# Optimization experiments

Measured on AMD Instinct MI355X. Metric: run time of the kernel, lower is better.

## Reference

```python
import jax, jax.numpy as jnp
import numpy as np

ANCHOR_STRIDE = 16
BASE_SIZE = 16
RATIOS = np.array([0.5, 1.0, 2.0])
SCALES = np.array([8.0, 16.0, 32.0])
RPN_NEG = 0.3
RPN_POS = 0.7
RPN_BATCH = 256
FG_FRAC = 0.5


def _generate_anchors():
    w = h = float(BASE_SIZE)
    cx = cy = 0.5 * (BASE_SIZE - 1)
    size = w * h
    ws = np.round(np.sqrt(size / RATIOS))
    hs = np.round(ws * RATIOS)
    out = []
    for wi, hi in zip(ws, hs):
        wss = wi * SCALES
        hss = hi * SCALES
        out.append(np.stack([cx - 0.5 * (wss - 1), cy - 0.5 * (hss - 1),
                             cx + 0.5 * (wss - 1), cy + 0.5 * (hss - 1)], 1))
    return np.concatenate(out, 0).astype(np.float32)  # [9, 4]


def _all_anchors(height, width):
    anchors = _generate_anchors()  # [A,4]
    sx = np.arange(width) * ANCHOR_STRIDE
    sy = np.arange(height) * ANCHOR_STRIDE
    SX, SY = np.meshgrid(sx, sy)  # 'xy' -> [H,W], row-major y then x
    shifts = np.stack([SX.ravel(), SY.ravel(), SX.ravel(), SY.ravel()], 1).astype(np.float32)  # [K,4]
    return (shifts[:, None, :] + anchors[None, :, :]).reshape(-1, 4), anchors.shape[0]  # [K*A,4], A


def _iou(a, g):
    # a: [N,4], g: [G,4]; +1 pixel convention
    area_a = (a[:, 2] - a[:, 0] + 1.0) * (a[:, 3] - a[:, 1] + 1.0)
    area_g = (g[:, 2] - g[:, 0] + 1.0) * (g[:, 3] - g[:, 1] + 1.0)
    iw = jnp.clip(jnp.minimum(a[:, None, 2], g[None, :, 2]) - jnp.maximum(a[:, None, 0], g[None, :, 0]) + 1.0, 0.0)
    ih = jnp.clip(jnp.minimum(a[:, None, 3], g[None, :, 3]) - jnp.maximum(a[:, None, 1], g[None, :, 1]) + 1.0, 0.0)
    inter = iw * ih  # [N,G]
    return inter / (area_a[:, None] + area_g[None, :] - inter)


def _bbox_transform(a, g):
    aw = a[:, 2] - a[:, 0] + 1.0
    ah = a[:, 3] - a[:, 1] + 1.0
    acx = a[:, 0] + 0.5 * (aw - 1.0)
    acy = a[:, 1] + 0.5 * (ah - 1.0)
    gw = g[:, 2] - g[:, 0] + 1.0
    gh = g[:, 3] - g[:, 1] + 1.0
    gcx = g[:, 0] + 0.5 * (gw - 1.0)
    gcy = g[:, 1] + 0.5 * (gh - 1.0)
    return jnp.stack([(gcx - acx) / aw, (gcy - acy) / ah, jnp.log(gw / aw), jnp.log(gh / ah)], 1)


def setup_inputs() -> dict:
    key = jax.random.key(0)
    B, G, H, W = 32, 50, 64, 64
    img = ANCHOR_STRIDE * H  # 1024
    k1, k2, k3, k4 = jax.random.split(key, 4)
    x1 = jax.random.uniform(k1, (B * G,)) * (img - 224.0)
    y1 = jax.random.uniform(k2, (B * G,)) * (img - 224.0)
    bw = 16.0 + jax.random.uniform(k3, (B * G,)) * 180.0
    bh = 16.0 + jax.random.uniform(k4, (B * G,)) * 180.0
    gt_bbox = jnp.stack([x1, y1, x1 + bw, y1 + bh], 1)
    return {"gt_bbox": gt_bbox, "batch_size": B, "n_gt": G, "height": H, "width": W}


def reference(gt_bbox, batch_size, n_gt, height, width):
    all_a, A = _all_anchors(height, width)
    img_w = ANCHOR_STRIDE * width
    img_h = ANCHOR_STRIDE * height
    inside = np.where((all_a[:, 0] >= 0) & (all_a[:, 1] >= 0) &
                      (all_a[:, 2] < img_w) & (all_a[:, 3] < img_h))[0]
    anc = jnp.asarray(all_a[inside])  # [N,4], static subset
    N = len(inside)
    NUM_FG = int(FG_FRAC * RPN_BATCH)
    gt = gt_bbox.reshape(batch_size, n_gt, 4)

    def subsample(mask, num_keep, k):
        # keep a random subset of size <= num_keep among mask==True
        pri = jnp.where(mask, jax.random.uniform(k, (N,)), jnp.inf)
        order = jnp.argsort(pri)
        rank = jnp.zeros((N,), jnp.int32).at[order].set(jnp.arange(N, dtype=jnp.int32))
        return mask & (rank < num_keep)

    def per_image(gt_b, key):
        ov = _iou(anc, gt_b)                 # [N,G]
        max_ov = ov.max(1)
        arg = ov.argmax(1)
        gt_max = ov.max(0)                   # [G]
        labels = jnp.full((N,), -1.0)
        labels = jnp.where(max_ov < RPN_NEG, 0.0, labels)
        labels = jnp.where(max_ov >= RPN_POS, 1.0, labels)
        # anchors achieving per-gt max overlap (for gts with positive overlap)
        gt_arg_hit = ((ov == gt_max[None, :]) & (gt_max[None, :] > 0)).any(1)
        labels = jnp.where(gt_arg_hit, 1.0, labels)
        kf, kb = jax.random.split(key)
        fg = labels == 1.0
        keep_fg = subsample(fg, NUM_FG, kf)
        labels = jnp.where(fg & ~keep_fg, -1.0, labels)
        num_bg = RPN_BATCH - keep_fg.sum()
        bg = labels == 0.0
        keep_bg = subsample(bg, num_bg, kb)
        labels = jnp.where(bg & ~keep_bg, -1.0, labels)
        reg = _bbox_transform(anc, gt_b[arg]) * jnp.clip(labels, 0.0)[:, None]
        return labels, reg

    keys = jax.random.split(jax.random.key(42), batch_size)
    labels, reg = jax.vmap(per_image)(gt, keys)  # [B,N], [B,N,4]

    KA = all_a.shape[0]
    all_labels = jnp.full((batch_size, KA), -1.0).at[:, inside].set(labels)
    all_reg = jnp.zeros((batch_size, KA, 4)).at[:, inside].set(reg)
    all_labels = all_labels.reshape(batch_size, height, width, A).transpose(0, 3, 1, 2)
    all_reg = all_reg.reshape(batch_size, height, width, A * 4).transpose(0, 3, 1, 2)
    return all_labels, all_reg
```

## Files before the change

### kernel.cpp

```cpp
#include <hip/hip_runtime.h>

#pragma clang fp contract(off)

#define BB 32
#define GG 50
#define AA 9
#define HH 64
#define WW 64
#define KAT (HH*WW*AA)
#define NCAP 23552
#define MAXC 4096
#define NUMFG 128
#define RPNB 256
#define BG_T 0.05f
#define LAB_SZ (BB*AA*HH*WW)
#define NGTB (BB*GG)
#define NMSKB 72
#define NPREPB (KAT/256)
#define NBLK4 23

__constant__ float c_aw[9] = {184.f,368.f,736.f,128.f,256.f,512.f, 88.f,176.f,352.f};
__constant__ float c_ah[9] = { 96.f,192.f,384.f,128.f,256.f,512.f,176.f,352.f,704.f};
__constant__ int c_xlo[9] = {6,11,23,4,8,16,3,5,11};
__constant__ int c_xhi[9] = {57,52,40,59,55,47,60,58,52};
__constant__ int c_nx [9] = {52,42,18,56,48,32,58,54,42};
__constant__ int c_ylo[9] = {3,6,12,4,8,16,5,11,22};
__constant__ int c_yhi[9] = {60,57,51,59,55,47,58,52,41};
__constant__ int c_ny [9] = {58,52,40,56,48,32,54,42,20};
__constant__ int c_pb[9] = {0,3072,6144,7168,11264,14336,15360,19456,22528};
__constant__ int c_fb[9] = {0,3,6,7,11,14,15,19,22};
__constant__ int c_bt4[NBLK4] = {0,0,0,1,1,1,2,3,3,3,3,4,4,4,5,6,6,6,6,7,7,7,8};

__device__ __forceinline__ unsigned rotl32(unsigned v, int d) {
  return (v << d) | (v >> (32 - d));
}

__device__ __forceinline__ void tf2x32(unsigned k0, unsigned k1,
                                       unsigned x0, unsigned x1,
                                       unsigned &o0, unsigned &o1) {
  unsigned ks2 = k0 ^ k1 ^ 0x1BD11BDAu;
  x0 += k0; x1 += k1;
#define TF_R(r) { x0 += x1; x1 = rotl32(x1, (r)); x1 ^= x0; }
  TF_R(13) TF_R(15) TF_R(26) TF_R(6)
  x0 += k1;  x1 += ks2 + 1u;
  TF_R(17) TF_R(29) TF_R(16) TF_R(24)
  x0 += ks2; x1 += k0 + 2u;
  TF_R(13) TF_R(15) TF_R(26) TF_R(6)
  x0 += k0;  x1 += k1 + 3u;
  TF_R(17) TF_R(29) TF_R(16) TF_R(24)
  x0 += k1;  x1 += ks2 + 4u;
  TF_R(13) TF_R(15) TF_R(26) TF_R(6)
  x0 += ks2; x1 += k0 + 5u;
#undef TF_R
  o0 = x0; o1 = x1;
}

__device__ __forceinline__ float bits_to_uniform(unsigned bits) {
  return __uint_as_float((bits >> 9) | 0x3f800000u) - 1.0f;
}

__device__ __forceinline__ float pri_uniform(unsigned k0, unsigned k1, int i) {
  unsigned o0, o1;
  tf2x32(k0, k1, 0u, (unsigned)i, o0, o1);
  return bits_to_uniform(o0 ^ o1);
}

__device__ __forceinline__ void box_from_ayx(int a, int x, int y,
                                             float &ax1, float &ay1, float &ax2, float &ay2) {
  float hw = 0.5f * (c_aw[a] - 1.0f);
  float hh = 0.5f * (c_ah[a] - 1.0f);
  float cx = (float)(16 * x) + 7.5f;
  float cy = (float)(16 * y) + 7.5f;
  ax1 = cx - hw; ay1 = cy - hh; ax2 = cx + hw; ay2 = cy + hh;
}

__device__ __forceinline__ void divmod_nx(int t, int rc, int &q, int &rm) {
  switch (t) {
    case 0: q = rc / 52; rm = rc - q * 52; break;
    case 1: q = rc / 42; rm = rc - q * 42; break;
    case 2: q = rc / 18; rm = rc - q * 18; break;
    case 3: q = rc / 56; rm = rc - q * 56; break;
    case 4: q = rc / 48; rm = rc - q * 48; break;
    case 5: q = rc / 32; rm = rc - q * 32; break;
    case 6: q = rc / 58; rm = rc - q * 58; break;
    case 7: q = rc / 54; rm = rc - q * 54; break;
    default: q = rc / 42; rm = rc - q * 42; break;
  }
}

__global__ void __launch_bounds__(256) k_pg(
    const float* __restrict__ gt,
    unsigned* __restrict__ keyf, unsigned* __restrict__ keyb,
    int* __restrict__ fg_cnt, int* __restrict__ bg_cnt,
    float* __restrict__ gt_max, unsigned long long* __restrict__ gmask,
    int* __restrict__ iref_j) {
  if (blockIdx.x == NGTB) {
    if (threadIdx.x < BB) {
      int b = threadIdx.x;
      fg_cnt[b] = 0; bg_cnt[b] = 0;
      unsigned h, l, f0, f1, g0, g1;
      tf2x32(0u, 42u, 0u, (unsigned)b, h, l);
      tf2x32(h, l, 0u, 0u, f0, f1);
      tf2x32(h, l, 0u, 1u, g0, g1);
      keyf[2*b] = f0; keyf[2*b+1] = f1;
      keyb[2*b] = g0; keyb[2*b+1] = g1;
    }
    return;
  }
  if (blockIdx.x > NGTB && blockIdx.x <= NGTB + NMSKB) {
    int idx = blockIdx.x - NGTB - 1;
    int pair = idx * 4 + (threadIdx.x >> 6);
    int b = pair / AA, t = pair % AA;
    int y = threadIdx.x & 63;
    float hh = 0.5f * (c_ah[t] - 1.0f);
    float cy = (float)(16 * y) + 7.5f;
    float ay1 = cy - hh, ay2 = cy + hh;
    unsigned long long m = 0;
    for (int g = 0; g < GG; ++g) {
      float gy1 = gt[(b * GG + g) * 4 + 1];
      float gy2 = gt[(b * GG + g) * 4 + 3];
      float ih = (fminf(ay2, gy2) - fmaxf(ay1, gy1)) + 1.0f;
      if (ih > 0.0f) m |= (1ull << g);
    }
    gmask[(b * AA + t) * 64 + y] = m;
    return;
  }
  if (blockIdx.x > NGTB + NMSKB) {
    int ka = (blockIdx.x - NGTB - 1 - NMSKB) * 256 + threadIdx.x;
    int a = ka % AA, pos = ka / AA, x = pos & 63, y = pos >> 6;
    int pre = 0; bool mine = false;
#pragma unroll
    for (int tt = 0; tt < 9; ++tt) {
      int xlo = c_xlo[tt], xhi = c_xhi[tt], ylo = c_ylo[tt], yhi = c_yhi[tt];
      int rb = min(y, yhi + 1) - ylo; rb = max(rb, 0);
      pre += c_nx[tt] * rb;
      if (y >= ylo && y <= yhi) {
        int cb = min(x, xhi + 1) - xlo; cb = max(cb, 0);
        pre += cb;
        bool ins = (x >= xlo) && (x <= xhi);
        if (ins && tt < a) pre++;
        if (tt == a) mine = ins;
      }
    }
    if (mine) {
      int j = c_pb[a] + (y - c_ylo[a]) * c_nx[a] + (x - c_xlo[a]);
      iref_j[j] = pre;
    }
    return;
  }
  int b = blockIdx.x / GG, g = blockIdx.x % GG;
  const float* gr = gt + (b * GG + g) * 4;
  float gx1 = gr[0], gy1 = gr[1], gx2 = gr[2], gy2 = gr[3];
  float gar = ((gx2 - gx1) + 1.0f) * ((gy2 - gy1) + 1.0f);
  int lane = threadIdx.x & 63, wv = threadIdx.x >> 6;
  float best = 0.0f;
#pragma unroll
  for (int t = 0; t < 9; ++t) {
    float hw = 0.5f * (c_aw[t] - 1.0f), hh = 0.5f * (c_ah[t] - 1.0f);
    int x0 = max(c_xlo[t], (int)floorf((gx1 - 8.5f - hw) * 0.0625f) - 1);
    int x1 = min(c_xhi[t], (int)ceilf ((gx2 - 6.5f + hw) * 0.0625f) + 1);
    int y0 = max(c_ylo[t], (int)floorf((gy1 - 8.5f - hh) * 0.0625f) - 1);
    int y1 = min(c_yhi[t], (int)ceilf ((gy2 - 6.5f + hh) * 0.0625f) + 1);
    if (x1 < x0 || y1 < y0) continue;
    int x = min(x0 + lane, x1);
    float cx = (float)(16 * x) + 7.5f;
    float ax1 = cx - hw, ax2 = cx + hw;
    float aarv = ((ax2 - ax1) + 1.0f) * ((hh + hh) + 1.0f);
    float iw = (fminf(ax2, gx2) - fmaxf(ax1, gx1)) + 1.0f; iw = fmaxf(iw, 0.0f);
    for (int y = y0 + wv; y <= y1; y += 4) {
      float cy = (float)(16 * y) + 7.5f;
      float ay1 = cy - hh, ay2 = cy + hh;
      float ih = (fminf(ay2, gy2) - fmaxf(ay1, gy1)) + 1.0f; ih = fmaxf(ih, 0.0f);
      float inter = iw * ih;
      best = fmaxf(best, inter / ((aarv + gar) - inter));
    }
  }
  for (int off = 32; off > 0; off >>= 1)
    best = fmaxf(best, __shfl_down(best, off));
  __shared__ float red[4];
  if (lane == 0) red[wv] = best;
  __syncthreads();
  if (threadIdx.x == 0)
    gt_max[b * GG + g] = fmaxf(fmaxf(red[0], red[1]), fmaxf(red[2], red[3]));
}

__global__ void __launch_bounds__(256) k_labels(
    const float* __restrict__ gt, const float* __restrict__ gt_max,
    const unsigned long long* __restrict__ gmask, const int* __restrict__ iref_j,
    const unsigned* __restrict__ keyf, const unsigned* __restrict__ keyb,
    signed char* __restrict__ lab, unsigned char* __restrict__ am,
    int* __restrict__ fg_cnt, unsigned long long* __restrict__ fg_key, int* __restrict__ fg_j,
    int* __restrict__ bg_cnt, unsigned long long* __restrict__ bg_key, int* __restrict__ bg_j) {
  __shared__ float4 sbox[GG];
  __shared__ float2 sga[GG];
  __shared__ unsigned long long s_gm[64];
  __shared__ unsigned long long s_fgk[1024]; __shared__ int s_fgj[1024];
  __shared__ unsigned long long s_bgk[1024]; __shared__ int s_bgj[1024];
  __shared__ int s_fgc, s_bgc, s_fgbase, s_bgbase;
  int b = blockIdx.y;
  int t = c_bt4[blockIdx.x];
  if (threadIdx.x == 0) { s_fgc = 0; s_bgc = 0; }
  if (threadIdx.x < GG) {
    float4 gbx = ((const float4*)(gt + b * GG * 4))[threadIdx.x];
    sbox[threadIdx.x] = gbx;
    float gar = ((gbx.z - gbx.x) + 1.0f) * ((gbx.w - gbx.y) + 1.0f);
    float m = gt_max[b * GG + threadIdx.x];
    sga[threadIdx.x] = make_float2(gar, (m > 0.0f) ? m : -1.0f);
  }
  if (threadIdx.x >= 64 && threadIdx.x < 128)
    s_gm[threadIdx.x - 64] = gmask[(b * AA + t) * 64 + (threadIdx.x - 64)];
  __syncthreads();

  int nx = c_nx[t];
  int nxny = nx * c_ny[t];
  int lane = threadIdx.x & 63, wv = threadIdx.x >> 6;
  int wstart = (blockIdx.x - c_fb[t]) * 1024 + wv * 256;

  float AX1[4], AY1[4], AX2[4], AY2[4], AV[4], BEST[4];
  int ARG[4]; bool ACT[4], HIT[4];
#pragma unroll
  for (int k = 0; k < 4; ++k) {
    int r = wstart + k * 64 + lane;
    ACT[k] = r < nxny;
    int rc = min(r, nxny - 1);
    int yy, xx; divmod_nx(t, rc, yy, xx);
    box_from_ayx(t, c_xlo[t] + xx, c_ylo[t] + yy, AX1[k], AY1[k], AX2[k], AY2[k]);
    AV[k] = ((AX2[k] - AX1[k]) + 1.0f) * ((AY2[k] - AY1[k]) + 1.0f);
    BEST[k] = 0.0f; ARG[k] = 0; HIT[k] = false;
  }

  unsigned long long m = 0;
  if (wstart < nxny) {
    int y0, y1, dum;
    divmod_nx(t, wstart, y0, dum);
    divmod_nx(t, min(wstart + 255, nxny - 1), y1, dum);
    int yy = y0 + lane;
    unsigned long long rowm = (yy <= y1) ? s_gm[c_ylo[t] + yy] : 0ull;
    unsigned lo = (unsigned)rowm, hi = (unsigned)(rowm >> 32);
    for (int off = 32; off > 0; off >>= 1) {
      lo |= (unsigned)__shfl_xor((int)lo, off);
      hi |= (unsigned)__shfl_xor((int)hi, off);
    }
    unsigned mlo = (unsigned)__builtin_amdgcn_readfirstlane((int)lo);
    unsigned mhi = (unsigned)__builtin_amdgcn_readfirstlane((int)hi);
    m = (((unsigned long long)mhi << 32) | (unsigned long long)mlo)
        & ((1ull << GG) - 1ull);
  }

  if (m) {
    int g = __builtin_ctzll(m); m &= m - 1;
    float4 gb = sbox[g]; float2 ga = sga[g];
    for (;;) {
      bool more = (m != 0ull);
      int g2 = 0; float4 gb2 = gb; float2 ga2 = ga;
      if (more) {
        g2 = __builtin_ctzll(m); m &= m - 1;
        gb2 = sbox[g2]; ga2 = sga[g2];
      }
#pragma unroll
      for (int k = 0; k < 4; ++k) {
        float iw = (fminf(AX2[k], gb.z) - fmaxf(AX1[k], gb.x)) + 1.0f; iw = fmaxf(iw, 0.0f);
        float ih = (fminf(AY2[k], gb.w) - fmaxf(AY1[k], gb.y)) + 1.0f; ih = fmaxf(ih, 0.0f);
        float inter = iw * ih;
        float ov = inter / ((AV[k] + ga.x) - inter);
        if (ov > BEST[k]) { BEST[k] = ov; ARG[k] = g; }
        HIT[k] = HIT[k] || (ov == ga.y);
      }
      if (!more) break;
      g = g2; gb = gb2; ga = ga2;
    }
  }

#pragma unroll
  for (int k = 0; k < 4; ++k) {
    int label = (HIT[k] || BEST[k] >= 0.7f) ? 1 : ((BEST[k] < 0.3f) ? 0 : -1);
    int j = c_pb[t] + wstart + k * 64 + lane;
    if (ACT[k]) {
      lab[b * NCAP + j] = (signed char)label;
      am[b * NCAP + j]  = (unsigned char)ARG[k];
    }
    int ir = ACT[k] ? iref_j[j] : 0;
    bool wf = ACT[k] && (label == 1);
    unsigned long long mf = __ballot(wf);
    if (mf) {
      int ldr = __builtin_ctzll(mf);
      int basew = 0;
      if (lane == ldr) basew = atomicAdd(&s_fgc, __popcll(mf));
      basew = __shfl(basew, ldr);
      if (wf) {
        float p = pri_uniform(keyf[2*b], keyf[2*b+1], ir);
        int pos = basew + __popcll(mf & ((1ull << lane) - 1ull));
        s_fgk[pos] = ((unsigned long long)__float_as_uint(p) << 32) | (unsigned)ir;
        s_fgj[pos] = j;
      }
    }
    float pb = 0.0f;
    bool wb = ACT[k] && (label == 0);
    if (wb) { pb = pri_uniform(keyb[2*b], keyb[2*b+1], ir); wb = (pb < BG_T); }
    unsigned long long mb = __ballot(wb);
    if (mb) {
      int ldr = __builtin_ctzll(mb);
      int basew = 0;
      if (lane == ldr) basew = atomicAdd(&s_bgc, __popcll(mb));
      basew = __shfl(basew, ldr);
      if (wb) {
        int pos = basew + __popcll(mb & ((1ull << lane) - 1ull));
        s_bgk[pos] = ((unsigned long long)__float_as_uint(pb) << 32) | (unsigned)ir;
        s_bgj[pos] = j;
      }
    }
  }
  __syncthreads();
  if (threadIdx.x == 0) s_fgbase = s_fgc ? atomicAdd(&fg_cnt[b], s_fgc) : 0;
  if (threadIdx.x == 64) s_bgbase = s_bgc ? atomicAdd(&bg_cnt[b], s_bgc) : 0;
  __syncthreads();
  for (int i = threadIdx.x; i < s_fgc; i += 256) {
    int pos = s_fgbase + i;
    if (pos < MAXC) { fg_key[b * MAXC + pos] = s_fgk[i]; fg_j[b * MAXC + pos] = s_fgj[i]; }
  }
  for (int i = threadIdx.x; i < s_bgc; i += 256) {
    int pos = s_bgbase + i;
    if (pos < MAXC) { bg_key[b * MAXC + pos] = s_bgk[i]; bg_j[b * MAXC + pos] = s_bgj[i]; }
  }
}

__global__ void __launch_bounds__(1024) k_select(
    const int* __restrict__ fg_cnt, const unsigned long long* __restrict__ fg_key,
    const int* __restrict__ fg_j,
    const int* __restrict__ bg_cnt, const unsigned long long* __restrict__ bg_key,
    const int* __restrict__ bg_j,
    signed char* __restrict__ lab) {
  __shared__ unsigned long long sk[MAXC];
  __shared__ int sj[MAXC];
  int b = blockIdx.x & (BB - 1);
  if (blockIdx.x < BB) {
    int F = min(fg_cnt[b], MAXC);
    if (F <= NUMFG) return;
    for (int c = threadIdx.x; c < F; c += blockDim.x) {
      sk[c] = fg_key[b * MAXC + c]; sj[c] = fg_j[b * MAXC + c];
    }
    __syncthreads();
    for (int c = threadIdx.x; c < F; c += blockDim.x) {
      unsigned long long me = sk[c];
      int rank = 0;
      for (int jx = 0; jx < F; ++jx) rank += (sk[jx] < me) ? 1 : 0;
      if (rank >= NUMFG) lab[b * NCAP + sj[c]] = -1;
    }
  } else {
    int nk = RPNB - min(fg_cnt[b], NUMFG);
    int C = min(bg_cnt[b], MAXC);
    for (int c = threadIdx.x; c < C; c += blockDim.x) {
      sk[c] = bg_key[b * MAXC + c]; sj[c] = bg_j[b * MAXC + c];
    }
    __syncthreads();
    for (int c = threadIdx.x; c < C; c += blockDim.x) {
      unsigned long long me = sk[c];
      int rank = 0;
      for (int jx = 0; jx < C; ++jx) rank += (sk[jx] < me) ? 1 : 0;
      if (rank < nk) lab[b * NCAP + sj[c]] = 2;
    }
  }
}

__global__ void k_out(const float* __restrict__ gt,
                      const signed char* __restrict__ lab, const unsigned char* __restrict__ am,
                      float* __restrict__ out) {
  int b = blockIdx.y;
  int t = blockIdx.x * 256 + threadIdx.x;
  int a = t >> 12, pos = t & 4095;
  int y = pos >> 6, x = pos & 63;
  int j = -1;
  if (x >= c_xlo[a] && x <= c_xhi[a] && y >= c_ylo[a] && y <= c_yhi[a])
    j = c_pb[a] + (y - c_ylo[a]) * c_nx[a] + (x - c_xlo[a]);
  float lv = -1.0f, t0 = 0.f, t1 = 0.f, t2 = 0.f, t3 = 0.f;
  if (j >= 0) {
    signed char v = lab[b * NCAP + j];
    lv = (v == 1) ? 1.0f : ((v == 2) ? 0.0f : -1.0f);
    if (v == 1) {
      float ax1, ay1, ax2, ay2;
      box_from_ayx(a, x, y, ax1, ay1, ax2, ay2);
      int g = am[b * NCAP + j];
      const float* gr = gt + (b * GG + g) * 4;
      float gx1 = gr[0], gy1 = gr[1], gx2 = gr[2], gy2 = gr[3];
      float aw = (ax2 - ax1) + 1.0f, ah = (ay2 - ay1) + 1.0f;
      float acx = ax1 + 0.5f * (aw - 1.0f), acy = ay1 + 0.5f * (ah - 1.0f);
      float gw = (gx2 - gx1) + 1.0f, gh = (gy2 - gy1) + 1.0f;
      float gcx = gx1 + 0.5f * (gw - 1.0f), gcy = gy1 + 0.5f * (gh - 1.0f);
      t0 = (gcx - acx) / aw;
      t1 = (gcy - acy) / ah;
      t2 = logf(gw / aw);
      t3 = logf(gh / ah);
    }
  }
  out[b * KAT + t] = lv;
  float* rb = out + LAB_SZ + b * (4 * KAT) + (a * 4) * 4096 + pos;
  rb[0] = t0; rb[4096] = t1; rb[2 * 4096] = t2; rb[3 * 4096] = t3;
}

extern "C" void kernel_launch(void* const* d_in, const int* in_sizes, int n_in,
                              void* d_out, int out_size, void* d_ws, size_t ws_size,
                              hipStream_t stream) {
  const float* gt = (const float*)d_in[0];
  float* out = (float*)d_out;

  char* w = (char*)d_ws;
  unsigned long long* fg_key = (unsigned long long*)w; w += BB*MAXC*8;
  unsigned long long* bg_key = (unsigned long long*)w; w += BB*MAXC*8;
  unsigned long long* gmask  = (unsigned long long*)w; w += BB*AA*64*8;
  int* iref_j      = (int*)w;            w += NCAP*sizeof(int);
  int* fg_cnt      = (int*)w;            w += 256;
  int* bg_cnt      = (int*)w;            w += 256;
  unsigned* keyf   = (unsigned*)w;       w += 256;
  unsigned* keyb   = (unsigned*)w;       w += 256;
  float* gt_max    = (float*)w;          w += ((BB*GG*4 + 255)/256)*256;
  int* fg_j        = (int*)w;            w += BB*MAXC*sizeof(int);
  int* bg_j        = (int*)w;            w += BB*MAXC*sizeof(int);
  signed char* lab = (signed char*)w;    w += BB*NCAP;
  unsigned char* am= (unsigned char*)w;  w += BB*NCAP;

  k_pg<<<NGTB + 1 + NMSKB + NPREPB, 256, 0, stream>>>(gt, keyf, keyb, fg_cnt, bg_cnt,
                                                      gt_max, gmask, iref_j);
  k_labels<<<dim3(NBLK4, BB), 256, 0, stream>>>(gt, gt_max, gmask, iref_j, keyf, keyb,
                                                lab, am, fg_cnt, fg_key, fg_j,
                                                bg_cnt, bg_key, bg_j);
  k_select<<<2*BB, 1024, 0, stream>>>(fg_cnt, fg_key, fg_j, bg_cnt, bg_key, bg_j, lab);
  k_out<<<dim3(KAT/256, BB), 256, 0, stream>>>(gt, lab, am, out);
}
```

Before: 150.9 us.

## Fuse four pipeline kernels into one cooperative persistent kernel with grid syncs

Replaces four separate kernel launches with a single cooperative persistent kernel of 1024 blocks. Each stage runs as a role over virtual block indices and the stages are separated by grid.sync(), which removes launch gaps between kernels. The select stage also moves from 64 blocks of 1024 threads to 256 blocks of 256 threads, each block ranking a quarter of the candidates, and drops the shared index array. The fused kernel holds a fixed 32KB of shared memory per block, which can limit occupancy, and a fallback to separate launches runs if the cooperative launch fails.

```diff
diff --git a/kernel.cpp b/kernel.cpp
--- a/kernel.cpp
+++ b/kernel.cpp
@@ -1,6 +1,9 @@
 #include <hip/hip_runtime.h>
+#include <hip/hip_cooperative_groups.h>
 
 #pragma clang fp contract(off)
+
+namespace cg = cooperative_groups;
 
 #define BB 32
 #define GG 50
@@ -18,6 +21,13 @@
 #define NMSKB 72
 #define NPREPB (KAT/256)
 #define NBLK4 23
+#define NV0 (NGTB + 1 + NMSKB + NPREPB)
+#define NV1 (NBLK4*BB)
+#define NV2 (BB*8)
+#define NV3 ((KAT/256)*BB)
+#define GRID 1024
+#define LBL_SMEM 26304
+#define SEL_SMEM 32768
 
 __constant__ float c_aw[9] = {184.f,368.f,736.f,128.f,256.f,512.f, 88.f,176.f,352.f};
 __constant__ float c_ah[9] = { 96.f,192.f,384.f,128.f,256.f,512.f,176.f,352.f,704.f};
@@ -88,13 +98,11 @@
   }
 }
 
-__global__ void __launch_bounds__(256) k_pg(
-    const float* __restrict__ gt,
-    unsigned* __restrict__ keyf, unsigned* __restrict__ keyb,
-    int* __restrict__ fg_cnt, int* __restrict__ bg_cnt,
-    float* __restrict__ gt_max, unsigned long long* __restrict__ gmask,
-    int* __restrict__ iref_j) {
-  if (blockIdx.x == NGTB) {
+
+__device__ __forceinline__ void role_p0(int vb, const float* __restrict__ gt,
+    unsigned* keyf, unsigned* keyb, int* fg_cnt, int* bg_cnt,
+    float* gt_max, unsigned long long* gmask, int* iref_j, char* smem) {
+  if (vb == NGTB) {
     if (threadIdx.x < BB) {
       int b = threadIdx.x;
       fg_cnt[b] = 0; bg_cnt[b] = 0;
@@ -107,8 +115,8 @@
     }
     return;
   }
-  if (blockIdx.x > NGTB && blockIdx.x <= NGTB + NMSKB) {
-    int idx = blockIdx.x - NGTB - 1;
+  if (vb > NGTB && vb <= NGTB + NMSKB) {
+    int idx = vb - NGTB - 1;
     int pair = idx * 4 + (threadIdx.x >> 6);
     int b = pair / AA, t = pair % AA;
     int y = threadIdx.x & 63;
@@ -125,8 +133,8 @@
     gmask[(b * AA + t) * 64 + y] = m;
     return;
   }
-  if (blockIdx.x > NGTB + NMSKB) {
-    int ka = (blockIdx.x - NGTB - 1 - NMSKB) * 256 + threadIdx.x;
+  if (vb > NGTB + NMSKB) {
+    int ka = (vb - NGTB - 1 - NMSKB) * 256 + threadIdx.x;
     int a = ka % AA, pos = ka / AA, x = pos & 63, y = pos >> 6;
     int pre = 0; bool mine = false;
 #pragma unroll
@@ -148,7 +156,7 @@
     }
     return;
   }
-  int b = blockIdx.x / GG, g = blockIdx.x % GG;
+  int b = vb / GG, g = vb % GG;
   const float* gr = gt + (b * GG + g) * 4;
   float gx1 = gr[0], gy1 = gr[1], gx2 = gr[2], gy2 = gr[3];
   float gar = ((gx2 - gx1) + 1.0f) * ((gy2 - gy1) + 1.0f);
@@ -177,29 +185,32 @@
   }
   for (int off = 32; off > 0; off >>= 1)
     best = fmaxf(best, __shfl_down(best, off));
-  __shared__ float red[4];
+  float* red = (float*)smem;
   if (lane == 0) red[wv] = best;
   __syncthreads();
   if (threadIdx.x == 0)
     gt_max[b * GG + g] = fmaxf(fmaxf(red[0], red[1]), fmaxf(red[2], red[3]));
-}
-
-__global__ void __launch_bounds__(256) k_labels(
-    const float* __restrict__ gt, const float* __restrict__ gt_max,
-    const unsigned long long* __restrict__ gmask, const int* __restrict__ iref_j,
+  __syncthreads();
+}
+
+__device__ __forceinline__ void role_labels(int vb, const float* __restrict__ gt,
+    const float* __restrict__ gt_max, const unsigned long long* __restrict__ gmask,
+    const int* __restrict__ iref_j,
     const unsigned* __restrict__ keyf, const unsigned* __restrict__ keyb,
     signed char* __restrict__ lab, unsigned char* __restrict__ am,
-    int* __restrict__ fg_cnt, unsigned long long* __restrict__ fg_key, int* __restrict__ fg_j,
-    int* __restrict__ bg_cnt, unsigned long long* __restrict__ bg_key, int* __restrict__ bg_j) {
-  __shared__ float4 sbox[GG];
-  __shared__ float2 sga[GG];
-  __shared__ unsigned long long s_gm[64];
-  __shared__ unsigned long long s_fgk[1024]; __shared__ int s_fgj[1024];
-  __shared__ unsigned long long s_bgk[1024]; __shared__ int s_bgj[1024];
-  __shared__ int s_fgc, s_bgc, s_fgbase, s_bgbase;
-  int b = blockIdx.y;
-  int t = c_bt4[blockIdx.x];
-  if (threadIdx.x == 0) { s_fgc = 0; s_bgc = 0; }
+    int* fg_cnt, unsigned long long* fg_key, int* fg_j,
+    int* bg_cnt, unsigned long long* bg_key, int* bg_j, char* smem) {
+  int b = vb / NBLK4, bx = vb - b * NBLK4;
+  int t = c_bt4[bx];
+  float4* sbox = (float4*)smem;
+  float2* sga  = (float2*)(smem + 800);
+  unsigned long long* s_gm  = (unsigned long long*)(smem + 1200);
+  unsigned long long* s_fgk = (unsigned long long*)(smem + 1712);
+  int* s_fgj = (int*)(smem + 9904);
+  unsigned long long* s_bgk = (unsigned long long*)(smem + 14000);
+  int* s_bgj = (int*)(smem + 22192);
+  int* s_cnt = (int*)(smem + 26288);
+  if (threadIdx.x == 0) { s_cnt[0] = 0; s_cnt[1] = 0; }
   if (threadIdx.x < GG) {
     float4 gbx = ((const float4*)(gt + b * GG * 4))[threadIdx.x];
     sbox[threadIdx.x] = gbx;
@@ -211,10 +222,9 @@
     s_gm[threadIdx.x - 64] = gmask[(b * AA + t) * 64 + (threadIdx.x - 64)];
   __syncthreads();
 
-  int nx = c_nx[t];
-  int nxny = nx * c_ny[t];
+  int nxny = c_nx[t] * c_ny[t];
   int lane = threadIdx.x & 63, wv = threadIdx.x >> 6;
-  int wstart = (blockIdx.x - c_fb[t]) * 1024 + wv * 256;
+  int wstart = (bx - c_fb[t]) * 1024 + wv * 256;
 
   float AX1[4], AY1[4], AX2[4], AY2[4], AV[4], BEST[4];
   int ARG[4]; bool ACT[4], HIT[4];
@@ -285,7 +295,7 @@
     if (mf) {
       int ldr = __builtin_ctzll(mf);
       int basew = 0;
-      if (lane == ldr) basew = atomicAdd(&s_fgc, __popcll(mf));
+      if (lane == ldr) basew = atomicAdd(&s_cnt[0], __popcll(mf));
       basew = __shfl(basew, ldr);
       if (wf) {
         float p = pri_uniform(keyf[2*b], keyf[2*b+1], ir);
@@ -301,7 +311,7 @@
     if (mb) {
       int ldr = __builtin_ctzll(mb);
       int basew = 0;
-      if (lane == ldr) basew = atomicAdd(&s_bgc, __popcll(mb));
+      if (lane == ldr) basew = atomicAdd(&s_cnt[1], __popcll(mb));
       basew = __shfl(basew, ldr);
       if (wb) {
         int pos = basew + __popcll(mb & ((1ull << lane) - 1ull));
@@ -311,62 +321,62 @@
     }
   }
   __syncthreads();
-  if (threadIdx.x == 0) s_fgbase = s_fgc ? atomicAdd(&fg_cnt[b], s_fgc) : 0;
-  if (threadIdx.x == 64) s_bgbase = s_bgc ? atomicAdd(&bg_cnt[b], s_bgc) : 0;
-  __syncthreads();
-  for (int i = threadIdx.x; i < s_fgc; i += 256) {
-    int pos = s_fgbase + i;
+  if (threadIdx.x == 0) s_cnt[2] = s_cnt[0] ? atomicAdd(&fg_cnt[b], s_cnt[0]) : 0;
+  if (threadIdx.x == 64) s_cnt[3] = s_cnt[1] ? atomicAdd(&bg_cnt[b], s_cnt[1]) : 0;
+  __syncthreads();
+  int fgc = s_cnt[0], bgc = s_cnt[1], fgb = s_cnt[2], bgb = s_cnt[3];
+  for (int i = threadIdx.x; i < fgc; i += 256) {
+    int pos = fgb + i;
     if (pos < MAXC) { fg_key[b * MAXC + pos] = s_fgk[i]; fg_j[b * MAXC + pos] = s_fgj[i]; }
   }
-  for (int i = threadIdx.x; i < s_bgc; i += 256) {
-    int pos = s_bgbase + i;
+  for (int i = threadIdx.x; i < bgc; i += 256) {
+    int pos = bgb + i;
     if (pos < MAXC) { bg_key[b * MAXC + pos] = s_bgk[i]; bg_j[b * MAXC + pos] = s_bgj[i]; }
   }
-}
-
-__global__ void __launch_bounds__(1024) k_select(
+  __syncthreads();
+}
+
+__device__ __forceinline__ void role_select(int vb,
     const int* __restrict__ fg_cnt, const unsigned long long* __restrict__ fg_key,
     const int* __restrict__ fg_j,
     const int* __restrict__ bg_cnt, const unsigned long long* __restrict__ bg_key,
     const int* __restrict__ bg_j,
-    signed char* __restrict__ lab) {
-  __shared__ unsigned long long sk[MAXC];
-  __shared__ int sj[MAXC];
-  int b = blockIdx.x & (BB - 1);
-  if (blockIdx.x < BB) {
-    int F = min(fg_cnt[b], MAXC);
-    if (F <= NUMFG) return;
-    for (int c = threadIdx.x; c < F; c += blockDim.x) {
-      sk[c] = fg_key[b * MAXC + c]; sj[c] = fg_j[b * MAXC + c];
-    }
+    signed char* __restrict__ lab, char* smem) {
+  int img = vb >> 3, slot = vb & 7;
+  unsigned long long* sk = (unsigned long long*)smem;
+  if (slot < 4) {
+    int F = min(fg_cnt[img], MAXC);
+    if (F > NUMFG) {
+      for (int i = threadIdx.x; i < F; i += 256) sk[i] = fg_key[img * MAXC + i];
+      __syncthreads();
+      for (int c = slot * 256 + threadIdx.x; c < F; c += 1024) {
+        unsigned long long me = sk[c];
+        int rank = 0;
+        for (int jx = 0; jx < F; ++jx) rank += (sk[jx] < me) ? 1 : 0;
+        if (rank >= NUMFG) lab[img * NCAP + fg_j[img * MAXC + c]] = -1;
+      }
+    }
+  } else {
+    int sub = slot - 4;
+    int nk = RPNB - min(fg_cnt[img], NUMFG);
+    int C = min(bg_cnt[img], MAXC);
+    for (int i = threadIdx.x; i < C; i += 256) sk[i] = bg_key[img * MAXC + i];
     __syncthreads();
-    for (int c = threadIdx.x; c < F; c += blockDim.x) {
-      unsigned long long me = sk[c];
-      int rank = 0;
-      for (int jx = 0; jx < F; ++jx) rank += (sk[jx] < me) ? 1 : 0;
-      if (rank >= NUMFG) lab[b * NCAP + sj[c]] = -1;
-    }
-  } else {
-    int nk = RPNB - min(fg_cnt[b], NUMFG);
-    int C = min(bg_cnt[b], MAXC);
-    for (int c = threadIdx.x; c < C; c += blockDim.x) {
-      sk[c] = bg_key[b * MAXC + c]; sj[c] = bg_j[b * MAXC + c];
-    }
-    __syncthreads();
-    for (int c = threadIdx.x; c < C; c += blockDim.x) {
+    for (int c = sub * 256 + threadIdx.x; c < C; c += 1024) {
       unsigned long long me = sk[c];
       int rank = 0;
       for (int jx = 0; jx < C; ++jx) rank += (sk[jx] < me) ? 1 : 0;
-      if (rank < nk) lab[b * NCAP + sj[c]] = 2;
-    }
-  }
-}
-
-__global__ void k_out(const float* __restrict__ gt,
-                      const signed char* __restrict__ lab, const unsigned char* __restrict__ am,
-                      float* __restrict__ out) {
-  int b = blockIdx.y;
-  int t = blockIdx.x * 256 + threadIdx.x;
+      if (rank < nk) lab[img * NCAP + bg_j[img * MAXC + c]] = 2;
+    }
+  }
+  __syncthreads();
+}
+
+__device__ __forceinline__ void role_out(int vb, const float* __restrict__ gt,
+    const signed char* __restrict__ lab, const unsigned char* __restrict__ am,
+    float* __restrict__ out) {
+  int b = vb / (KAT/256), bx = vb - b * (KAT/256);
+  int t = bx * 256 + threadIdx.x;
   int a = t >> 12, pos = t & 4095;
   int y = pos >> 6, x = pos & 63;
   int j = -1;
@@ -397,6 +407,60 @@
   rb[0] = t0; rb[4096] = t1; rb[2 * 4096] = t2; rb[3 * 4096] = t3;
 }
 
+extern "C" __global__ void __launch_bounds__(256, 4) k_fused(
+    const float* __restrict__ gt, float* __restrict__ out,
+    unsigned* keyf, unsigned* keyb, int* fg_cnt, int* bg_cnt,
+    float* gt_max, unsigned long long* gmask, int* iref_j,
+    unsigned long long* fg_key, int* fg_j,
+    unsigned long long* bg_key, int* bg_j,
+    signed char* lab, unsigned char* am) {
+  cg::grid_group grid = cg::this_grid();
+  __shared__ __align__(16) char smem[SEL_SMEM];
+  for (int vb = blockIdx.x; vb < NV0; vb += GRID)
+    role_p0(vb, gt, keyf, keyb, fg_cnt, bg_cnt, gt_max, gmask, iref_j, smem);
+  grid.sync();
+  for (int vb = blockIdx.x; vb < NV1; vb += GRID)
+    role_labels(vb, gt, gt_max, gmask, iref_j, keyf, keyb, lab, am,
+                fg_cnt, fg_key, fg_j, bg_cnt, bg_key, bg_j, smem);
+  grid.sync();
+  for (int vb = blockIdx.x; vb < NV2; vb += GRID)
+    role_select(vb, fg_cnt, fg_key, fg_j, bg_cnt, bg_key, bg_j, lab, smem);
+  grid.sync();
+  for (int vb = blockIdx.x; vb < NV3; vb += GRID)
+    role_out(vb, gt, lab, am, out);
+}
+
+__global__ void __launch_bounds__(256) k_p0_fb(const float* __restrict__ gt,
+    unsigned* keyf, unsigned* keyb, int* fg_cnt, int* bg_cnt,
+    float* gt_max, unsigned long long* gmask, int* iref_j) {
+  __shared__ __align__(16) char smem[64];
+  role_p0(blockIdx.x, gt, keyf, keyb, fg_cnt, bg_cnt, gt_max, gmask, iref_j, smem);
+}
+__global__ void __launch_bounds__(256) k_lab_fb(const float* __restrict__ gt,
+    const float* __restrict__ gt_max, const unsigned long long* __restrict__ gmask,
+    const int* __restrict__ iref_j,
+    const unsigned* __restrict__ keyf, const unsigned* __restrict__ keyb,
+    signed char* lab, unsigned char* am,
+    int* fg_cnt, unsigned long long* fg_key, int* fg_j,
+    int* bg_cnt, unsigned long long* bg_key, int* bg_j) {
+  __shared__ __align__(16) char smem[LBL_SMEM];
+  role_labels(blockIdx.x, gt, gt_max, gmask, iref_j, keyf, keyb, lab, am,
+              fg_cnt, fg_key, fg_j, bg_cnt, bg_key, bg_j, smem);
+}
+__global__ void __launch_bounds__(256) k_sel_fb(
+    const int* __restrict__ fg_cnt, const unsigned long long* __restrict__ fg_key,
+    const int* __restrict__ fg_j,
+    const int* __restrict__ bg_cnt, const unsigned long long* __restrict__ bg_key,
+    const int* __restrict__ bg_j, signed char* lab) {
+  __shared__ __align__(16) char smem[SEL_SMEM];
+  role_select(blockIdx.x, fg_cnt, fg_key, fg_j, bg_cnt, bg_key, bg_j, lab, smem);
+}
+__global__ void __launch_bounds__(256) k_out_fb(const float* __restrict__ gt,
+    const signed char* __restrict__ lab, const unsigned char* __restrict__ am,
+    float* __restrict__ out) {
+  role_out(blockIdx.x, gt, lab, am, out);
+}
+
 extern "C" void kernel_launch(void* const* d_in, const int* in_sizes, int n_in,
                               void* d_out, int out_size, void* d_ws, size_t ws_size,
                               hipStream_t stream) {
@@ -418,11 +482,19 @@
   signed char* lab = (signed char*)w;    w += BB*NCAP;
   unsigned char* am= (unsigned char*)w;  w += BB*NCAP;
 
-  k_pg<<<NGTB + 1 + NMSKB + NPREPB, 256, 0, stream>>>(gt, keyf, keyb, fg_cnt, bg_cnt,
-                                                      gt_max, gmask, iref_j);
-  k_labels<<<dim3(NBLK4, BB), 256, 0, stream>>>(gt, gt_max, gmask, iref_j, keyf, keyb,
-                                                lab, am, fg_cnt, fg_key, fg_j,
-                                                bg_cnt, bg_key, bg_j);
-  k_select<<<2*BB, 1024, 0, stream>>>(fg_cnt, fg_key, fg_j, bg_cnt, bg_key, bg_j, lab);
-  k_out<<<dim3(KAT/256, BB), 256, 0, stream>>>(gt, lab, am, out);
-}
+  void* args[] = { (void*)&gt, (void*)&out, (void*)&keyf, (void*)&keyb,
+                   (void*)&fg_cnt, (void*)&bg_cnt, (void*)&gt_max, (void*)&gmask,
+                   (void*)&iref_j, (void*)&fg_key, (void*)&fg_j,
+                   (void*)&bg_key, (void*)&bg_j, (void*)&lab, (void*)&am };
+  hipError_t e = hipLaunchCooperativeKernel((void*)k_fused, dim3(GRID), dim3(256),
+                                            args, 0, stream);
+  if (e != hipSuccess) {
+    k_p0_fb<<<NV0, 256, 0, stream>>>(gt, keyf, keyb, fg_cnt, bg_cnt,
+                                     gt_max, gmask, iref_j);
+    k_lab_fb<<<NV1, 256, 0, stream>>>(gt, gt_max, gmask, iref_j, keyf, keyb,
+                                      lab, am, fg_cnt, fg_key, fg_j,
+                                      bg_cnt, bg_key, bg_j);
+    k_sel_fb<<<NV2, 256, 0, stream>>>(fg_cnt, fg_key, fg_j, bg_cnt, bg_key, bg_j, lab);
+    k_out_fb<<<NV3, 256, 0, stream>>>(gt, lab, am, out);
+  }
+}
```

New measurement: 466.5 us. 209% more time.

## Split per-image rank selection across eight 256-thread blocks per image

Applied to the files above, without the earlier changes.

k_select now launches eight 256-thread blocks per image instead of two 1024-thread blocks. Four blocks handle foreground and four handle background, and each covers a strided slice of candidates while every block reloads the full key array into shared memory. The j-index array is read from global memory only when a write is needed, which drops its shared copy. k_labels is also switched to a flattened 1D grid. The aim is to spread the quadratic rank loop over more CUs, at the cost of loading the keys four times per image.

```diff
diff --git a/kernel.cpp b/kernel.cpp
--- a/kernel.cpp
+++ b/kernel.cpp
@@ -18,6 +18,12 @@
 #define NMSKB 72
 #define NPREPB (KAT/256)
 #define NBLK4 23
+#define NV0 (NGTB + 1 + NMSKB + NPREPB)
+#define NV1 (NBLK4*BB)
+#define NV2 (BB*8)
+#define NV3 ((KAT/256)*BB)
+#define LBL_SMEM 26304
+#define SEL_SMEM 32768
 
 __constant__ float c_aw[9] = {184.f,368.f,736.f,128.f,256.f,512.f, 88.f,176.f,352.f};
 __constant__ float c_ah[9] = { 96.f,192.f,384.f,128.f,256.f,512.f,176.f,352.f,704.f};
@@ -197,8 +203,8 @@
   __shared__ unsigned long long s_fgk[1024]; __shared__ int s_fgj[1024];
   __shared__ unsigned long long s_bgk[1024]; __shared__ int s_bgj[1024];
   __shared__ int s_fgc, s_bgc, s_fgbase, s_bgbase;
-  int b = blockIdx.y;
-  int t = c_bt4[blockIdx.x];
+  int b = blockIdx.x / NBLK4, bx = blockIdx.x - b * NBLK4;
+  int t = c_bt4[bx];
   if (threadIdx.x == 0) { s_fgc = 0; s_bgc = 0; }
   if (threadIdx.x < GG) {
     float4 gbx = ((const float4*)(gt + b * GG * 4))[threadIdx.x];
@@ -211,10 +217,9 @@
     s_gm[threadIdx.x - 64] = gmask[(b * AA + t) * 64 + (threadIdx.x - 64)];
   __syncthreads();
 
-  int nx = c_nx[t];
-  int nxny = nx * c_ny[t];
+  int nxny = c_nx[t] * c_ny[t];
   int lane = threadIdx.x & 63, wv = threadIdx.x >> 6;
-  int wstart = (blockIdx.x - c_fb[t]) * 1024 + wv * 256;
+  int wstart = (bx - c_fb[t]) * 1024 + wv * 256;
 
   float AX1[4], AY1[4], AX2[4], AY2[4], AV[4], BEST[4];
   int ARG[4]; bool ACT[4], HIT[4];
@@ -324,47 +329,43 @@
   }
 }
 
-__global__ void __launch_bounds__(1024) k_select(
+__global__ void __launch_bounds__(256) k_select(
     const int* __restrict__ fg_cnt, const unsigned long long* __restrict__ fg_key,
     const int* __restrict__ fg_j,
     const int* __restrict__ bg_cnt, const unsigned long long* __restrict__ bg_key,
     const int* __restrict__ bg_j,
     signed char* __restrict__ lab) {
   __shared__ unsigned long long sk[MAXC];
-  __shared__ int sj[MAXC];
-  int b = blockIdx.x & (BB - 1);
-  if (blockIdx.x < BB) {
-    int F = min(fg_cnt[b], MAXC);
+  int img = blockIdx.x >> 3, slot = blockIdx.x & 7;
+  if (slot < 4) {
+    int F = min(fg_cnt[img], MAXC);
     if (F <= NUMFG) return;
-    for (int c = threadIdx.x; c < F; c += blockDim.x) {
-      sk[c] = fg_key[b * MAXC + c]; sj[c] = fg_j[b * MAXC + c];
-    }
+    for (int i = threadIdx.x; i < F; i += 256) sk[i] = fg_key[img * MAXC + i];
     __syncthreads();
-    for (int c = threadIdx.x; c < F; c += blockDim.x) {
+    for (int c = slot * 256 + threadIdx.x; c < F; c += 1024) {
       unsigned long long me = sk[c];
       int rank = 0;
       for (int jx = 0; jx < F; ++jx) rank += (sk[jx] < me) ? 1 : 0;
-      if (rank >= NUMFG) lab[b * NCAP + sj[c]] = -1;
+      if (rank >= NUMFG) lab[img * NCAP + fg_j[img * MAXC + c]] = -1;
     }
   } else {
-    int nk = RPNB - min(fg_cnt[b], NUMFG);
-    int C = min(bg_cnt[b], MAXC);
-    for (int c = threadIdx.x; c < C; c += blockDim.x) {
-      sk[c] = bg_key[b * MAXC + c]; sj[c] = bg_j[b * MAXC + c];
-    }
+    int sub = slot - 4;
+    int nk = RPNB - min(fg_cnt[img], NUMFG);
+    int C = min(bg_cnt[img], MAXC);
+    for (int i = threadIdx.x; i < C; i += 256) sk[i] = bg_key[img * MAXC + i];
     __syncthreads();
-    for (int c = threadIdx.x; c < C; c += blockDim.x) {
+    for (int c = sub * 256 + threadIdx.x; c < C; c += 1024) {
       unsigned long long me = sk[c];
       int rank = 0;
       for (int jx = 0; jx < C; ++jx) rank += (sk[jx] < me) ? 1 : 0;
-      if (rank < nk) lab[b * NCAP + sj[c]] = 2;
-    }
-  }
-}
-
-__global__ void k_out(const float* __restrict__ gt,
-                      const signed char* __restrict__ lab, const unsigned char* __restrict__ am,
-                      float* __restrict__ out) {
+      if (rank < nk) lab[img * NCAP + bg_j[img * MAXC + c]] = 2;
+    }
+  }
+}
+
+__global__ void __launch_bounds__(256) k_out(const float* __restrict__ gt,
+    const signed char* __restrict__ lab, const unsigned char* __restrict__ am,
+    float* __restrict__ out) {
   int b = blockIdx.y;
   int t = blockIdx.x * 256 + threadIdx.x;
   int a = t >> 12, pos = t & 4095;
@@ -418,11 +419,11 @@
   signed char* lab = (signed char*)w;    w += BB*NCAP;
   unsigned char* am= (unsigned char*)w;  w += BB*NCAP;
 
-  k_pg<<<NGTB + 1 + NMSKB + NPREPB, 256, 0, stream>>>(gt, keyf, keyb, fg_cnt, bg_cnt,
-                                                      gt_max, gmask, iref_j);
-  k_labels<<<dim3(NBLK4, BB), 256, 0, stream>>>(gt, gt_max, gmask, iref_j, keyf, keyb,
-                                                lab, am, fg_cnt, fg_key, fg_j,
-                                                bg_cnt, bg_key, bg_j);
-  k_select<<<2*BB, 1024, 0, stream>>>(fg_cnt, fg_key, fg_j, bg_cnt, bg_key, bg_j, lab);
+  k_pg<<<NV0, 256, 0, stream>>>(gt, keyf, keyb, fg_cnt, bg_cnt,
+                                gt_max, gmask, iref_j);
+  k_labels<<<NV1, 256, 0, stream>>>(gt, gt_max, gmask, iref_j, keyf, keyb,
+                                    lab, am, fg_cnt, fg_key, fg_j,
+                                    bg_cnt, bg_key, bg_j);
+  k_select<<<NV2, 256, 0, stream>>>(fg_cnt, fg_key, fg_j, bg_cnt, bg_key, bg_j, lab);
   k_out<<<dim3(KAT/256, BB), 256, 0, stream>>>(gt, lab, am, out);
 }
```

New measurement: 144.6 us. 4.2% less time.
